# Kernel tuning notes

Hardware: AMD Instinct MI355X
Metric: run time of the kernel (lower is better)

The kernel has to match this reference:

```python
import jax, jax.numpy as jnp
import numpy as np

N_TOKENS = 4096
HIDDEN = 1024
N_EXPERTS = 8
TOP_K = 2
EXPANDED = 2048


def setup_inputs() -> dict:
    key = jax.random.key(0)
    ks = jax.random.split(key, 4)
    tokens = jax.random.normal(ks[0], (N_TOKENS, HIDDEN), dtype=jnp.float32)
    router_w = jax.random.normal(ks[1], (N_EXPERTS, HIDDEN), dtype=jnp.float32) * (1.0 / np.sqrt(HIDDEN))
    router_b = jnp.zeros((N_EXPERTS,), dtype=jnp.float32)
    w1 = jax.random.normal(ks[2], (N_EXPERTS, HIDDEN, EXPANDED), dtype=jnp.float32) * (1.0 / np.sqrt(HIDDEN))
    b1 = jnp.zeros((N_EXPERTS, EXPANDED), dtype=jnp.float32)
    w2 = jax.random.normal(ks[3], (N_EXPERTS, EXPANDED, HIDDEN), dtype=jnp.float32) * (1.0 / np.sqrt(EXPANDED))
    b2 = jnp.zeros((N_EXPERTS, HIDDEN), dtype=jnp.float32)
    return {"tokens": tokens, "router_w": router_w, "router_b": router_b,
            "w1": w1, "b1": b1, "w2": w2, "b2": b2}


def reference(tokens, router_w, router_b, w1, b1, w2, b2):
    # Router: logits [N, E], top-k scores -> softmax over the k selected experts.
    logits = tokens @ router_w.T + router_b
    top_scores, expert_ids = jax.lax.top_k(logits, TOP_K)      # [N, K]
    probs = jax.nn.softmax(top_scores, axis=-1)                # [N, K]

    # Instead of gathering full per-token weight matrices (as the torch code does),
    # run each expert's dense MLP over all tokens and combine with the per-token
    # routing weight for that expert. Identical math: each token's contribution is
    # sum_k probs[n,k] * MLP_{expert_ids[n,k]}(tokens[n]).
    out = jnp.zeros_like(tokens)
    for e in range(N_EXPERTS):
        h = jax.nn.gelu(tokens @ w1[e] + b1[e], approximate=False)  # [N, EXPANDED]
        o = h @ w2[e] + b2[e]                                       # [N, HIDDEN]
        # Combined routing weight for expert e (top_k indices are distinct).
        gate = jnp.sum(jnp.where(expert_ids == e, probs, 0.0), axis=-1)  # [N]
        out = out + gate[:, None] * o
    return out
```

## Files before the change

### kernel.cpp

```cpp
#include <hip/hip_runtime.h>
#include <hip/hip_bf16.h>

typedef unsigned short u16;
typedef __attribute__((ext_vector_type(8))) short short8;
typedef __attribute__((ext_vector_type(4))) float f32x4;

#define N_TOKENS 4096
#define HIDDEN   1024
#define N_EXP    8
#define EXPAND   2048

#define TOKB_OFF  0ull
#define W1T_OFF   8388608ull
#define OBUF_OFF  8388608ull
#define W2T_OFF   41943040ull
#define H_OFF     75497472ull
#define RLT_OFF   109051904ull
#define RLG_OFF   109084672ull
#define CNT_OFF   109117440ull
#define E01_OFF   109117472ull
#define GATE_OFF  109183008ull
#define ROWS2_OFF 109215776ull

__device__ __forceinline__ u16 f2bf(float f) {
  union { float f; unsigned u; } v; v.f = f;
  unsigned r = v.u + 0x7fffu + ((v.u >> 16) & 1u);
  return (u16)(r >> 16);
}

__device__ __forceinline__ float bf2f(u16 b) {
  union { unsigned u; float f; } v; v.u = ((unsigned)b) << 16;
  return v.f;
}

__device__ __forceinline__ void glds16(const void* g, void* l) {
  __builtin_amdgcn_global_load_lds(
      (const __attribute__((address_space(1))) void*)g,
      (__attribute__((address_space(3))) void*)l, 16, 0, 0);
}

__device__ __forceinline__ float gelu_tanh(float x) {
  float u = x * (0.7978845608f + 0.0356774081f * x * x);
  float t = __expf(-2.0f * fabsf(u));
  float th = (1.0f - t) / (1.0f + t);
  th = (u >= 0.0f) ? th : -th;
  return 0.5f * x * (1.0f + th);
}

__global__ __launch_bounds__(256) void prep_k(const float* __restrict__ w1,
                                              u16* __restrict__ w1t,
                                              const float* __restrict__ w2,
                                              u16* __restrict__ w2t,
                                              const float* __restrict__ tokens,
                                              const float* __restrict__ rw,
                                              const float* __restrict__ rb,
                                              u16* __restrict__ tokb,
                                              int* __restrict__ e01,
                                              float* __restrict__ gates) {
  __shared__ __align__(16) char smem[32768];
  int x = blockIdx.x;
  int tid = threadIdx.x;

  if (x >= 1024) {
    u16 (*t)[66] = (u16 (*)[66])smem;
    int idx = x - 1024;
    const float* in; u16* out; int R, C, cx, ry, e;
    if (idx < 4096) {
      e = idx >> 9; int rem = idx & 511;
      cx = rem & 31; ry = rem >> 5;
      in = w1; out = w1t; R = HIDDEN; C = EXPAND;
    } else {
      int id2 = idx - 4096;
      e = id2 >> 9; int rem = id2 & 511;
      cx = rem & 15; ry = rem >> 4;
      in = w2; out = w2t; R = EXPAND; C = HIDDEN;
    }
    int c0 = cx * 64, r0 = ry * 64;
    const float* ip = in + (size_t)e * R * C;
    u16* op = out + (size_t)e * R * C;
    #pragma unroll
    for (int i = 0; i < 16; ++i) {
      int flat = i * 256 + tid;
      int row = flat >> 6, col = flat & 63;
      t[row][col] = f2bf(ip[(size_t)(r0 + row) * C + c0 + col]);
    }
    __syncthreads();
    #pragma unroll
    for (int i = 0; i < 16; ++i) {
      int flat = i * 256 + tid;
      int orow = flat >> 6, ocol = flat & 63;
      op[(size_t)(c0 + orow) * R + r0 + ocol] = t[ocol][orow];
    }
    return;
  }

  float* rwl = (float*)smem;
  for (int i = tid; i < N_EXP * HIDDEN / 4; i += 256)
    ((float4*)rwl)[i] = ((const float4*)rw)[i];
  __syncthreads();
  int w = tid >> 6, l = tid & 63;
  int t = x * 4 + w;
  const float* tp = tokens + (size_t)t * HIDDEN;
  u16* tb = tokb + (size_t)t * HIDDEN;
  float acc[8] = {0.f,0.f,0.f,0.f,0.f,0.f,0.f,0.f};
  #pragma unroll
  for (int it = 0; it < 4; ++it) {
    int k = it * 256 + l * 4;
    float4 tv = *(const float4*)&tp[k];
    ushort4 o;
    o.x = f2bf(tv.x); o.y = f2bf(tv.y); o.z = f2bf(tv.z); o.w = f2bf(tv.w);
    *(ushort4*)&tb[k] = o;
    #pragma unroll
    for (int e = 0; e < 8; ++e) {
      const float4 rv = *(const float4*)&rwl[e * HIDDEN + k];
      acc[e] += tv.x * rv.x + tv.y * rv.y + tv.z * rv.z + tv.w * rv.w;
    }
  }
  #pragma unroll
  for (int off = 32; off >= 1; off >>= 1) {
    #pragma unroll
    for (int e = 0; e < 8; ++e) acc[e] += __shfl_xor(acc[e], off);
  }
  if (l == 0) {
    float lg[8];
    #pragma unroll
    for (int e = 0; e < 8; ++e) lg[e] = acc[e] + rb[e];
    int b0 = 0; float v0 = lg[0];
    #pragma unroll
    for (int e = 1; e < 8; ++e) if (lg[e] > v0) { v0 = lg[e]; b0 = e; }
    int b1 = -1; float v1 = -3.4e38f;
    #pragma unroll
    for (int e = 0; e < 8; ++e) {
      if (e == b0) continue;
      if (lg[e] > v1) { v1 = lg[e]; b1 = e; }
    }
    float d = expf(v1 - v0);
    float p1 = d / (1.f + d);
    float p0 = 1.f - p1;
    e01[t * 2] = b0;   e01[t * 2 + 1] = b1;
    gates[t * 2] = p0; gates[t * 2 + 1] = p1;
  }
}

__global__ __launch_bounds__(1024) void order_k(const int* __restrict__ e01,
                                                const float* __restrict__ gates,
                                                int* __restrict__ cnt,
                                                int* __restrict__ rlt,
                                                float* __restrict__ rlg,
                                                int* __restrict__ rows2) {
  __shared__ int slotbuf[2 * N_TOKENS];
  __shared__ int wcnt[16][N_EXP];
  __shared__ int base_run[N_EXP];
  __shared__ int basep[N_EXP];
  int tid = threadIdx.x, w = tid >> 6, l = tid & 63;
  if (tid < N_EXP) base_run[tid] = 0;
  __syncthreads();
  unsigned long long ltmask = (1ull << l) - 1ull;
  #pragma unroll
  for (int c = 0; c < 8; ++c) {
    int i = c * 1024 + tid;
    int ei = e01[i];
    int myrank = 0;
    #pragma unroll
    for (int e = 0; e < N_EXP; ++e) {
      unsigned long long b = __ballot(ei == e);
      if (l == 0) wcnt[w][e] = __popcll(b);
      if (ei == e) myrank = __popcll(b & ltmask);
    }
    __syncthreads();
    if (tid < N_EXP) {
      int e = tid, off = base_run[e];
      #pragma unroll
      for (int ww = 0; ww < 16; ++ww) {
        int v = wcnt[ww][e]; wcnt[ww][e] = off; off += v;
      }
      base_run[e] = off;
    }
    __syncthreads();
    slotbuf[i] = wcnt[w][ei] + myrank;
    __syncthreads();
  }
  if (tid < N_EXP) cnt[tid] = base_run[tid];
  if (tid == 0) {
    int s = 0;
    for (int e = 0; e < N_EXP; ++e) { basep[e] = s; s += base_run[e]; }
  }
  __syncthreads();
  #pragma unroll
  for (int c = 0; c < 8; ++c) {
    int i = c * 1024 + tid;
    int e = e01[i];
    int row = basep[e] + slotbuf[i];
    rlt[row] = i >> 1;
    rlg[row] = gates[i];
    rows2[i] = row;
  }
}


#define STAGE(Ad, Bd, KT) {                                                      \
  glds16(ga[0] + (size_t)(KT) * 64, &Ad[threadIdx.x * 8]);                       \
  glds16(ga[1] + (size_t)(KT) * 64, &Ad[(512 + threadIdx.x) * 8]);               \
  glds16(gb0   + (size_t)(KT) * 64, &Bd[threadIdx.x * 8]);                       \
}

#define GEMM_TILE(As, Bs) {                                                      \
  _Pragma("unroll") for (int kk = 0; kk < 2; ++kk) {                             \
    short8 afr[2], bfr[2];                                                       \
    _Pragma("unroll") for (int i = 0; i < 2; ++i) {                              \
      afr[i] = *(const short8*)&As[oa[kk][i]];                                   \
      bfr[i] = *(const short8*)&Bs[ob[kk][i]];                                   \
    }                                                                            \
    _Pragma("unroll") for (int i = 0; i < 2; ++i)                                \
      _Pragma("unroll") for (int j = 0; j < 2; ++j)                              \
        acc[i][j] = __builtin_amdgcn_mfma_f32_16x16x32_bf16(                     \
            afr[i], bfr[j], acc[i][j], 0, 0, 0);                                 \
  }                                                                              \
}

#define FRAG_OFFSETS {                                                           \
  _Pragma("unroll") for (int kk = 0; kk < 2; ++kk) {                             \
    int cc = kk * 4 + lg;                                                        \
    _Pragma("unroll") for (int i = 0; i < 2; ++i) {                              \
      int Ra = wr * 32 + i * 16 + lr;                                            \
      oa[kk][i] = Ra * 64 + (cc ^ (Ra & 7)) * 8;                                 \
      int Rb = wc * 32 + i * 16 + lr;                                            \
      ob[kk][i] = Rb * 64 + (cc ^ (Rb & 7)) * 8;                                 \
    }                                                                            \
  }                                                                              \
}

__global__ __launch_bounds__(512) void ffn1_k(const u16* __restrict__ tok,
                                              const u16* __restrict__ w1t,
                                              const float* __restrict__ b1,
                                              const int* __restrict__ rlt,
                                              const int* __restrict__ cnt,
                                              u16* __restrict__ h) {
  __shared__ __align__(16) short A0[8192];
  __shared__ __align__(16) short A1[8192];
  __shared__ __align__(16) short B0[4096];
  __shared__ __align__(16) short B1[4096];

  int tid = threadIdx.x, w = tid >> 6, l = tid & 63;
  int wr = w >> 1, wc = w & 1;
  int lr = l & 15, lg = l >> 4;
  int oa[2][2], ob[2][2];
  FRAG_OFFSETS

  int e = blockIdx.x & 7;
  int rnk = blockIdx.x >> 3;
  int estr = gridDim.x >> 3;
  int m0 = 0;
  #pragma unroll
  for (int i = 0; i < 8; ++i) { int ci = cnt[i]; if (i < e) m0 += ci; }
  int ne = cnt[e];
  int mts = (ne + 127) >> 7;
  int NT_e = mts * (EXPAND / 64);

  for (int r = rnk; r < NT_e; r += estr) {
    int mt = r >> 5, nt = r & 31;
    int m0g = m0 + mt * 128;
    int mrem = ne - mt * 128;

    const u16* ga[2]; const u16* gb0;
    #pragma unroll
    for (int c = 0; c < 2; ++c) {
      int flat = c * 512 + tid, rih = flat >> 3;
      int ch = (flat & 7) ^ (rih & 7);
      int tokid = rlt[m0g + ((rih < mrem) ? rih : 0)];
      ga[c] = tok + (size_t)tokid * HIDDEN + ch * 8;
    }
    {
      int rih = tid >> 3;
      int ch = (tid & 7) ^ (rih & 7);
      int nrow = nt * 64 + rih;
      gb0 = w1t + (size_t)e * (EXPAND * HIDDEN) + (size_t)nrow * HIDDEN + ch * 8;
    }

    f32x4 acc[2][2] = {};
    STAGE(A0, B0, 0)
    __syncthreads();
    #pragma unroll 1
    for (int it = 0; it < 8; ++it) {
      STAGE(A1, B1, 2 * it + 1)
      GEMM_TILE(A0, B0)
      __syncthreads();
      if (it < 7) STAGE(A0, B0, 2 * it + 2)
      GEMM_TILE(A1, B1)
      __syncthreads();
    }

    #pragma unroll
    for (int i = 0; i < 2; ++i) {
      #pragma unroll
      for (int rr = 0; rr < 4; ++rr) {
        int row = wr * 32 + i * 16 + lg * 4 + rr;
        if (row >= mrem) continue;
        size_t hrow = (size_t)(m0g + row) * EXPAND;
        #pragma unroll
        for (int j = 0; j < 2; ++j) {
          int col = nt * 64 + wc * 32 + j * 16 + lr;
          float x = acc[i][j][rr] + b1[e * EXPAND + col];
          h[hrow + col] = f2bf(gelu_tanh(x));
        }
      }
    }
  }
}

__global__ __launch_bounds__(512) void ffn2_k(const u16* __restrict__ h,
                                              const u16* __restrict__ w2t,
                                              const float* __restrict__ b2,
                                              const float* __restrict__ rlg,
                                              const int* __restrict__ cnt,
                                              u16* __restrict__ obuf) {
  __shared__ __align__(16) short A0[8192];
  __shared__ __align__(16) short A1[8192];
  __shared__ __align__(16) short B0[4096];
  __shared__ __align__(16) short B1[4096];

  int tid = threadIdx.x, w = tid >> 6, l = tid & 63;
  int wr = w >> 1, wc = w & 1;
  int lr = l & 15, lg = l >> 4;
  int oa[2][2], ob[2][2];
  FRAG_OFFSETS

  int e = blockIdx.x & 7;
  int rnk = blockIdx.x >> 3;
  int estr = gridDim.x >> 3;
  int m0 = 0;
  #pragma unroll
  for (int i = 0; i < 8; ++i) { int ci = cnt[i]; if (i < e) m0 += ci; }
  int ne = cnt[e];
  int mts = (ne + 127) >> 7;
  int NT_e = mts * (HIDDEN / 64);

  for (int r = rnk; r < NT_e; r += estr) {
    int mt = r >> 4, nt = r & 15;
    int m0g = m0 + mt * 128;
    int mrem = ne - mt * 128;

    const u16* ga[2]; const u16* gb0;
    #pragma unroll
    for (int c = 0; c < 2; ++c) {
      int flat = c * 512 + tid, rih = flat >> 3;
      int ch = (flat & 7) ^ (rih & 7);
      int rowg = m0g + ((rih < mrem) ? rih : 0);
      ga[c] = h + (size_t)rowg * EXPAND + ch * 8;
    }
    {
      int rih = tid >> 3;
      int ch = (tid & 7) ^ (rih & 7);
      int nrow = nt * 64 + rih;
      gb0 = w2t + (size_t)e * (HIDDEN * EXPAND) + (size_t)nrow * EXPAND + ch * 8;
    }

    f32x4 acc[2][2] = {};
    STAGE(A0, B0, 0)
    __syncthreads();
    #pragma unroll 1
    for (int it = 0; it < 16; ++it) {
      STAGE(A1, B1, 2 * it + 1)
      GEMM_TILE(A0, B0)
      __syncthreads();
      if (it < 15) STAGE(A0, B0, 2 * it + 2)
      GEMM_TILE(A1, B1)
      __syncthreads();
    }

    #pragma unroll
    for (int i = 0; i < 2; ++i) {
      #pragma unroll
      for (int rr = 0; rr < 4; ++rr) {
        int row = wr * 32 + i * 16 + lg * 4 + rr;
        if (row >= mrem) continue;
        float gate = rlg[m0g + row];
        size_t orow = (size_t)(m0g + row) * HIDDEN;
        #pragma unroll
        for (int j = 0; j < 2; ++j) {
          int col = nt * 64 + wc * 32 + j * 16 + lr;
          obuf[orow + col] = f2bf((acc[i][j][rr] + b2[e * HIDDEN + col]) * gate);
        }
      }
    }
  }
}

__global__ __launch_bounds__(256) void combine_k(const u16* __restrict__ obuf,
                                                 const int* __restrict__ rows2,
                                                 float* __restrict__ out) {
  int t = blockIdx.x, c = threadIdx.x;
  int r0 = rows2[t * 2], r1 = rows2[t * 2 + 1];
  ushort4 a = ((const ushort4*)obuf)[(size_t)r0 * 256 + c];
  ushort4 b = ((const ushort4*)obuf)[(size_t)r1 * 256 + c];
  float4 o;
  o.x = bf2f(a.x) + bf2f(b.x);
  o.y = bf2f(a.y) + bf2f(b.y);
  o.z = bf2f(a.z) + bf2f(b.z);
  o.w = bf2f(a.w) + bf2f(b.w);
  ((float4*)out)[(size_t)t * 256 + c] = o;
}

extern "C" void kernel_launch(void* const* d_in, const int* in_sizes, int n_in,
                              void* d_out, int out_size, void* d_ws, size_t ws_size,
                              hipStream_t stream) {
  const float* tokens   = (const float*)d_in[0];
  const float* router_w = (const float*)d_in[1];
  const float* router_b = (const float*)d_in[2];
  const float* w1       = (const float*)d_in[3];
  const float* b1       = (const float*)d_in[4];
  const float* w2       = (const float*)d_in[5];
  const float* b2       = (const float*)d_in[6];
  float* out = (float*)d_out;

  char* ws = (char*)d_ws;
  u16*   tokb  = (u16*)(ws + TOKB_OFF);
  u16*   w1t   = (u16*)(ws + W1T_OFF);
  u16*   obuf  = (u16*)(ws + OBUF_OFF);
  u16*   w2t   = (u16*)(ws + W2T_OFF);
  u16*   h     = (u16*)(ws + H_OFF);
  int*   rlt   = (int*)(ws + RLT_OFF);
  float* rlg   = (float*)(ws + RLG_OFF);
  int*   cnt   = (int*)(ws + CNT_OFF);
  int*   e01   = (int*)(ws + E01_OFF);
  float* gates = (float*)(ws + GATE_OFF);
  int*   rows2 = (int*)(ws + ROWS2_OFF);

  prep_k<<<9216, 256, 0, stream>>>(w1, w1t, w2, w2t,
                                   tokens, router_w, router_b, tokb, e01, gates);
  order_k<<<1, 1024, 0, stream>>>(e01, gates, cnt, rlt, rlg, rows2);
  ffn1_k<<<2048, 512, 0, stream>>>(tokb, w1t, b1, rlt, cnt, h);
  ffn2_k<<<1024, 512, 0, stream>>>(h, w2t, b2, rlg, cnt, obuf);
  combine_k<<<N_TOKENS, 256, 0, stream>>>(obuf, rows2, out);
}
```

Baseline: 198.2 us.

## Split single-block routing sort into parallel count, scan, scatter kernels

Replaces the single-workgroup order_k, which loops serially over 8 chunks with several barriers each, with three kernels: a 32-block per-expert count, a one-thread scan producing per-block output bases, and a 32-block scatter using ballot-based ranks. The aim is to spread the routing sort across multiple CUs and drop the serial chunk loop. In exchange it adds two extra kernel launches, and the scan runs on a single thread.

```diff
diff --git a/kernel.cpp b/kernel.cpp
--- a/kernel.cpp
+++ b/kernel.cpp
@@ -21,6 +21,8 @@
 #define E01_OFF   109117472ull
 #define GATE_OFF  109183008ull
 #define ROWS2_OFF 109215776ull
+#define BCNT_OFF  109248544ull
+#define OBASE_OFF 109249568ull
 
 __device__ __forceinline__ u16 f2bf(float f) {
   union { float f; unsigned u; } v; v.f = f;
@@ -142,59 +144,67 @@
   }
 }
 
-__global__ __launch_bounds__(1024) void order_k(const int* __restrict__ e01,
-                                                const float* __restrict__ gates,
-                                                int* __restrict__ cnt,
-                                                int* __restrict__ rlt,
-                                                float* __restrict__ rlg,
-                                                int* __restrict__ rows2) {
-  __shared__ int slotbuf[2 * N_TOKENS];
-  __shared__ int wcnt[16][N_EXP];
-  __shared__ int base_run[N_EXP];
-  __shared__ int basep[N_EXP];
-  int tid = threadIdx.x, w = tid >> 6, l = tid & 63;
-  if (tid < N_EXP) base_run[tid] = 0;
+__global__ __launch_bounds__(256) void sortcnt_k(const int* __restrict__ e01,
+                                                 int* __restrict__ bcnt) {
+  __shared__ int wc[4][8];
+  int b = blockIdx.x, tid = threadIdx.x, w = tid >> 6, l = tid & 63;
+  int ei = e01[b * 256 + tid];
+  #pragma unroll
+  for (int e = 0; e < 8; ++e) {
+    unsigned long long m = __ballot(ei == e);
+    if (l == 0) wc[w][e] = __popcll(m);
+  }
   __syncthreads();
-  unsigned long long ltmask = (1ull << l) - 1ull;
-  #pragma unroll
-  for (int c = 0; c < 8; ++c) {
-    int i = c * 1024 + tid;
-    int ei = e01[i];
-    int myrank = 0;
-    #pragma unroll
-    for (int e = 0; e < N_EXP; ++e) {
-      unsigned long long b = __ballot(ei == e);
-      if (l == 0) wcnt[w][e] = __popcll(b);
-      if (ei == e) myrank = __popcll(b & ltmask);
-    }
-    __syncthreads();
-    if (tid < N_EXP) {
-      int e = tid, off = base_run[e];
-      #pragma unroll
-      for (int ww = 0; ww < 16; ++ww) {
-        int v = wcnt[ww][e]; wcnt[ww][e] = off; off += v;
-      }
-      base_run[e] = off;
-    }
-    __syncthreads();
-    slotbuf[i] = wcnt[w][ei] + myrank;
-    __syncthreads();
-  }
-  if (tid < N_EXP) cnt[tid] = base_run[tid];
-  if (tid == 0) {
+  if (tid < 8)
+    bcnt[tid * 32 + b] = wc[0][tid] + wc[1][tid] + wc[2][tid] + wc[3][tid];
+}
+
+__global__ void scan_k(const int* __restrict__ bcnt,
+                       int* __restrict__ obase, int* __restrict__ cnt) {
+  if (threadIdx.x == 0) {
+    int ec[8];
+    for (int e = 0; e < 8; ++e) {
+      int s = 0;
+      for (int b = 0; b < 32; ++b) { obase[e * 32 + b] = s; s += bcnt[e * 32 + b]; }
+      ec[e] = s; cnt[e] = s;
+    }
+    int base = 0;
+    for (int e = 0; e < 8; ++e) {
+      for (int b = 0; b < 32; ++b) obase[e * 32 + b] += base;
+      base += ec[e];
+    }
+  }
+}
+
+__global__ __launch_bounds__(256) void scatter_k(const int* __restrict__ e01,
+                                                 const float* __restrict__ gates,
+                                                 const int* __restrict__ obase,
+                                                 int* __restrict__ rlt,
+                                                 float* __restrict__ rlg,
+                                                 int* __restrict__ rows2) {
+  __shared__ int wc[4][8];
+  __shared__ int wpre[4][8];
+  int b = blockIdx.x, tid = threadIdx.x, w = tid >> 6, l = tid & 63;
+  int i = b * 256 + tid;
+  int ei = e01[i];
+  unsigned long long ltm = (1ull << l) - 1ull;
+  int lanerank = 0;
+  #pragma unroll
+  for (int e = 0; e < 8; ++e) {
+    unsigned long long m = __ballot(ei == e);
+    if (l == 0) wc[w][e] = __popcll(m);
+    if (ei == e) lanerank = __popcll(m & ltm);
+  }
+  __syncthreads();
+  if (tid < 8) {
     int s = 0;
-    for (int e = 0; e < N_EXP; ++e) { basep[e] = s; s += base_run[e]; }
+    for (int ww = 0; ww < 4; ++ww) { wpre[ww][tid] = s; s += wc[ww][tid]; }
   }
   __syncthreads();
-  #pragma unroll
-  for (int c = 0; c < 8; ++c) {
-    int i = c * 1024 + tid;
-    int e = e01[i];
-    int row = basep[e] + slotbuf[i];
-    rlt[row] = i >> 1;
-    rlg[row] = gates[i];
-    rows2[i] = row;
-  }
+  int row = obase[ei * 32 + b] + wpre[w][ei] + lanerank;
+  rlt[row] = i >> 1;
+  rlg[row] = gates[i];
+  rows2[i] = row;
 }
 
 
@@ -425,10 +435,14 @@
   int*   e01   = (int*)(ws + E01_OFF);
   float* gates = (float*)(ws + GATE_OFF);
   int*   rows2 = (int*)(ws + ROWS2_OFF);
+  int*   bcnt  = (int*)(ws + BCNT_OFF);
+  int*   obase = (int*)(ws + OBASE_OFF);
 
   prep_k<<<9216, 256, 0, stream>>>(w1, w1t, w2, w2t,
                                    tokens, router_w, router_b, tokb, e01, gates);
-  order_k<<<1, 1024, 0, stream>>>(e01, gates, cnt, rlt, rlg, rows2);
+  sortcnt_k<<<32, 256, 0, stream>>>(e01, bcnt);
+  scan_k<<<1, 64, 0, stream>>>(bcnt, obase, cnt);
+  scatter_k<<<32, 256, 0, stream>>>(e01, gates, obase, rlt, rlg, rows2);
   ffn1_k<<<2048, 512, 0, stream>>>(tokb, w1t, b1, rlt, cnt, h);
   ffn2_k<<<1024, 512, 0, stream>>>(h, w2t, b2, rlg, cnt, obuf);
   combine_k<<<N_TOKENS, 256, 0, stream>>>(obuf, rows2, out);
```

After: 193.7 us. 2.3% less time.
